# Kernel optimization log

Measured on AMD Instinct MI355X. Metric: run time of the kernel, lower is better.

The kernel has to match this reference:

```python
import jax, jax.numpy as jnp
import numpy as np

N0 = 4096
C = 128
DEPTH = 3
RATIO = 0.5
AVG_DEG = 32
BN_EPS = 1e-5


def setup_inputs() -> dict:
    key = jax.random.key(0)
    ks = jax.random.split(key, 6)
    x = jax.random.normal(ks[0], (N0, C), dtype=jnp.float32)
    # sparse symmetric adjacency (avg degree ~AVG_DEG), no self loops, dense layout
    mask = jax.random.bernoulli(ks[1], AVG_DEG / N0, (N0, N0)).astype(jnp.float32)
    adj = jnp.maximum(mask, mask.T) * (1.0 - jnp.eye(N0, dtype=jnp.float32))
    scale = 1.0 / np.sqrt(C)
    conv_w = jax.random.normal(ks[2], (2 * DEPTH + 1, C, C), dtype=jnp.float32) * scale
    conv_b = jax.random.normal(ks[3], (2 * DEPTH + 1, C), dtype=jnp.float32) * 0.01
    pool_w = jax.random.normal(ks[4], (DEPTH, C), dtype=jnp.float32)
    bn_g = jnp.ones((2 * DEPTH + 1, C), dtype=jnp.float32)
    bn_b = jnp.zeros((2 * DEPTH + 1, C), dtype=jnp.float32)
    return {"x": x, "adj": adj, "conv_w": conv_w, "conv_b": conv_b,
            "pool_w": pool_w, "bn_g": bn_g, "bn_b": bn_b}


def _gcn(x, A, W, b):
    # GCNConv(improved=True): A_hat = A + 2I, symmetric deg normalization
    n = A.shape[0]
    Ah = A + 2.0 * jnp.eye(n, dtype=A.dtype)
    deg = Ah.sum(axis=1)
    d_safe = jnp.where(deg > 0, deg, 1.0)
    dn = jnp.where(deg > 0, jax.lax.rsqrt(d_safe), 0.0)
    An = dn[:, None] * Ah * dn[None, :]
    return An @ (x @ W) + b


def _bn(x, g, b):
    # BatchNorm1d, training mode (biased variance)
    m = x.mean(axis=0)
    v = x.var(axis=0)
    return g * (x - m) * jax.lax.rsqrt(v + BN_EPS) + b


def _augment(A):
    # add_self_loops -> spspmm(A,A) -> remove_self_loops, done densely
    n = A.shape[0]
    I = jnp.eye(n, dtype=A.dtype)
    Aa = A + I
    return (Aa @ Aa) * (1.0 - I)


def _topk_pool(x, A, p):
    score = jnp.tanh((x @ p) / jnp.linalg.norm(p))
    k = int(np.ceil(RATIO * x.shape[0]))
    vals, perm = jax.lax.top_k(score, k)
    xn = x[perm] * vals[:, None]
    An = A[perm][:, perm]
    return xn, An, perm


def reference(x, adj, conv_w, conv_b, pool_w, bn_g, bn_b):
    x = x.astype(jnp.float32)
    x = _bn(jax.nn.relu(_gcn(x, adj, conv_w[0], conv_b[0])), bn_g[0], bn_b[0])
    xs, adjs, perms = [x], [adj], []
    A = adj
    for i in range(1, DEPTH + 1):
        A2 = _augment(A)
        x, A, perm = _topk_pool(x, A2, pool_w[i - 1])
        x = _bn(jax.nn.relu(_gcn(x, A, conv_w[i], conv_b[i])), bn_g[i], bn_b[i])
        if i < DEPTH:
            xs.append(x)
            adjs.append(A)
        perms.append(perm)
    for i in range(DEPTH):
        j = DEPTH - 1 - i
        res, Aj, perm = xs[j], adjs[j], perms[j]
        up = jnp.zeros_like(res).at[perm].set(x)
        x = res + up  # sum_res=True
        x = _gcn(x, Aj, conv_w[DEPTH + 1 + i], conv_b[DEPTH + 1 + i])
        if i < DEPTH - 1:
            x = jax.nn.relu(x)
        x = _bn(x, bn_g[DEPTH + 1 + i], bn_b[DEPTH + 1 + i])
    return x
```

## Files before the change

### kernel.cpp

```cpp
#include <hip/hip_runtime.h>
#include <cstdint>
#include <cstddef>

typedef __bf16 bf16;
typedef __bf16 bf16x8 __attribute__((ext_vector_type(8)));
typedef __bf16 bf16x4 __attribute__((ext_vector_type(4)));
typedef float floatx4 __attribute__((ext_vector_type(4)));
typedef int   intx4  __attribute__((ext_vector_type(4)));
typedef short shortx8 __attribute__((ext_vector_type(8)));
typedef char  cx8    __attribute__((ext_vector_type(8)));

#define GLD16(gp, lp) __builtin_amdgcn_global_load_lds( \
    (const __attribute__((address_space(1))) void*)(gp), \
    (__attribute__((address_space(3))) void*)(lp), 16, 0, 0)

__global__ __launch_bounds__(256) void gemm_sym_i8(
    const char* __restrict__ R, short* __restrict__ Cs16, int* __restrict__ Cs32,
    int n , int kIters, int G, int pairs)
{
  __shared__ __align__(16) char As[128 * 64];
  __shared__ __align__(16) char Bs[128 * 64];

  const int pair = blockIdx.x;
  int rem = pair, bm = 0;
  while (rem >= G - bm) { rem -= G - bm; ++bm; }
  const int bn = bm + rem;
  const int m0 = bm * 128;
  const int n0 = bn * 128;

  const int t = threadIdx.x;
  const int w = t >> 6, l = t & 63;
  const int wr = w >> 1, wc = w & 1;
  const int lr = l & 15, q = l >> 4;
  const int k0base = blockIdx.y * kIters * 64;

  const char* Ab = R + (size_t)m0 * n + k0base;
  const char* Bb = R + (size_t)n0 * n + k0base;
  const int srow = t >> 2;
  const int schunk = (t & 3) * 16;

  intx4 acc[4][4];
#pragma unroll
  for (int i = 0; i < 4; ++i)
#pragma unroll
    for (int j = 0; j < 4; ++j) acc[i][j] = (intx4)0;

  for (int kb = 0; kb < kIters; ++kb) {
    const int k0 = kb * 64;
    __syncthreads();
    GLD16(Ab + (size_t)srow * n + k0 + schunk,        As + (size_t)t * 16);
    GLD16(Ab + (size_t)(srow + 64) * n + k0 + schunk, As + (size_t)(t + 256) * 16);
    GLD16(Bb + (size_t)srow * n + k0 + schunk,        Bs + (size_t)t * 16);
    GLD16(Bb + (size_t)(srow + 64) * n + k0 + schunk, Bs + (size_t)(t + 256) * 16);
    __syncthreads();

    intx4 af[4], bfr[4];
#pragma unroll
    for (int mi = 0; mi < 4; ++mi)
      af[mi] = *(const intx4*)&As[(wr * 64 + mi * 16 + lr) * 64 + q * 16];
#pragma unroll
    for (int ni = 0; ni < 4; ++ni)
      bfr[ni] = *(const intx4*)&Bs[(wc * 64 + ni * 16 + lr) * 64 + q * 16];
#pragma unroll
    for (int mi = 0; mi < 4; ++mi)
#pragma unroll
      for (int ni = 0; ni < 4; ++ni)
        acc[mi][ni] = __builtin_amdgcn_mfma_i32_16x16x64_i8(
            af[mi], bfr[ni], acc[mi][ni], 0, 0, 0);
  }

  const size_t so = ((size_t)blockIdx.y * pairs + pair) * 16384;
#pragma unroll
  for (int mi = 0; mi < 4; ++mi)
#pragma unroll
    for (int ni = 0; ni < 4; ++ni) {
      const int cl = wc * 64 + ni * 16 + lr;
      const int rb = wr * 64 + mi * 16 + q * 4;
#pragma unroll
      for (int r = 0; r < 4; ++r) {
        int v = acc[mi][ni][r];
        if (Cs16) Cs16[so + (size_t)(rb + r) * 128 + cl] = (short)v;
        else      Cs32[so + (size_t)(rb + r) * 128 + cl] = v;
      }
    }
}

__global__ void sym_post_i(const short* __restrict__ Cs16, const int* __restrict__ Cs32,
                           bf16* __restrict__ Abf, float* __restrict__ Af,
                           int k, int G, int pairs, int nz)
{
  int rem = blockIdx.x, bm = 0;
  while (rem >= G - bm) { rem -= G - bm; ++bm; }
  const int bn = bm + rem;
  const int t = threadIdx.x;
  const int i = t >> 1;
  const int jc = blockIdx.y * 16 + (t & 1) * 8;
  const int r = bm * 128 + i;
  const size_t sbase = (size_t)blockIdx.x * 16384 + (size_t)i * 128 + jc;

  int v[8];
#pragma unroll
  for (int e = 0; e < 8; ++e) v[e] = 0;
  for (int z = 0; z < nz; ++z) {
    const size_t off = sbase + (size_t)z * pairs * 16384;
    if (Cs16) {
      shortx8 a = *(const shortx8*)&Cs16[off];
#pragma unroll
      for (int e = 0; e < 8; ++e) v[e] += (int)a[e];
    } else {
      intx4 a0 = *(const intx4*)&Cs32[off];
      intx4 a1 = *(const intx4*)&Cs32[off + 4];
#pragma unroll
      for (int e = 0; e < 4; ++e) { v[e] += a0[e]; v[e + 4] += a1[e]; }
    }
  }
#pragma unroll
  for (int e = 0; e < 8; ++e) {
    const int c = bn * 128 + jc + e;
    const float val = (c == r) ? 0.0f : (float)v[e];
    if (Abf) Abf[(size_t)r * k + c] = (bf16)val;
    if (Af)  Af[(size_t)r * k + c] = val;
    if (bm != bn) {
      if (Abf) Abf[(size_t)c * k + r] = (bf16)val;
      if (Af)  Af[(size_t)c * k + r] = val;
    }
  }
}

__global__ __launch_bounds__(256) void gemm_sym(
    const bf16* __restrict__ R, bf16* __restrict__ CsBf, float* __restrict__ CsF,
    int n , int kIters, int G, int pairs)
{
  __shared__ __align__(16) bf16 As[128 * 32];
  __shared__ __align__(16) bf16 Bs[128 * 32];

  const int pair = blockIdx.x;
  int rem = pair, bm = 0;
  while (rem >= G - bm) { rem -= G - bm; ++bm; }
  const int bn = bm + rem;
  const int m0 = bm * 128;
  const int n0 = bn * 128;

  const int t = threadIdx.x;
  const int w = t >> 6, l = t & 63;
  const int wr = w >> 1, wc = w & 1;
  const int lr = l & 15, q = l >> 4;
  const int k0base = blockIdx.y * kIters * 32;

  const bf16* Ab = R + (size_t)m0 * n + k0base;
  const bf16* Bb = R + (size_t)n0 * n + k0base;
  const int srow = t >> 2;
  const int schunk = (t & 3) * 8;

  floatx4 acc[4][4];
#pragma unroll
  for (int i = 0; i < 4; ++i)
#pragma unroll
    for (int j = 0; j < 4; ++j) acc[i][j] = (floatx4)0.0f;

  for (int kb = 0; kb < kIters; ++kb) {
    const int k0 = kb * 32;
    __syncthreads();
    GLD16(Ab + (size_t)srow * n + k0 + schunk,        As + (size_t)t * 8);
    GLD16(Ab + (size_t)(srow + 64) * n + k0 + schunk, As + (size_t)(t + 256) * 8);
    GLD16(Bb + (size_t)srow * n + k0 + schunk,        Bs + (size_t)t * 8);
    GLD16(Bb + (size_t)(srow + 64) * n + k0 + schunk, Bs + (size_t)(t + 256) * 8);
    __syncthreads();

    bf16x8 af[4], bfr[4];
#pragma unroll
    for (int mi = 0; mi < 4; ++mi)
      af[mi] = *(const bf16x8*)&As[(wr * 64 + mi * 16 + lr) * 32 + q * 8];
#pragma unroll
    for (int ni = 0; ni < 4; ++ni)
      bfr[ni] = *(const bf16x8*)&Bs[(wc * 64 + ni * 16 + lr) * 32 + q * 8];
#pragma unroll
    for (int mi = 0; mi < 4; ++mi)
#pragma unroll
      for (int ni = 0; ni < 4; ++ni)
        acc[mi][ni] = __builtin_amdgcn_mfma_f32_16x16x32_bf16(
            af[mi], bfr[ni], acc[mi][ni], 0, 0, 0);
  }

  const size_t so = ((size_t)blockIdx.y * pairs + pair) * 16384;
#pragma unroll
  for (int mi = 0; mi < 4; ++mi)
#pragma unroll
    for (int ni = 0; ni < 4; ++ni) {
      const int cl = wc * 64 + ni * 16 + lr;
      const int rb = wr * 64 + mi * 16 + q * 4;
#pragma unroll
      for (int r = 0; r < 4; ++r) {
        float v = acc[mi][ni][r];
        if (CsBf) CsBf[so + (size_t)(rb + r) * 128 + cl] = (bf16)v;
        else      CsF[so + (size_t)(rb + r) * 128 + cl] = v;
      }
    }
}

__global__ void sym_post(const bf16* __restrict__ CsBf, const float* __restrict__ CsF,
                         bf16* __restrict__ Abf, float* __restrict__ Af,
                         int k, int G, int pairs, int nz)
{
  int rem = blockIdx.x, bm = 0;
  while (rem >= G - bm) { rem -= G - bm; ++bm; }
  const int bn = bm + rem;
  const int t = threadIdx.x;
  const int i = t >> 1;
  const int jc = blockIdx.y * 16 + (t & 1) * 8;
  const int r = bm * 128 + i;
  const size_t sbase = (size_t)blockIdx.x * 16384 + (size_t)i * 128 + jc;

  float v[8];
#pragma unroll
  for (int e = 0; e < 8; ++e) v[e] = 0.0f;
  for (int z = 0; z < nz; ++z) {
    const size_t off = sbase + (size_t)z * pairs * 16384;
    if (CsBf) {
      bf16x8 a = *(const bf16x8*)&CsBf[off];
#pragma unroll
      for (int e = 0; e < 8; ++e) v[e] += (float)a[e];
    } else {
#pragma unroll
      for (int e = 0; e < 8; e += 4) {
        floatx4 a = *(const floatx4*)&CsF[off + e];
#pragma unroll
        for (int j = 0; j < 4; ++j) v[e + j] += a[j];
      }
    }
  }
#pragma unroll
  for (int e = 0; e < 8; ++e) {
    const int c = bn * 128 + jc + e;
    const float val = (c == r) ? 0.0f : v[e];
    if (Abf) Abf[(size_t)r * k + c] = (bf16)val;
    if (Af)  Af[(size_t)r * k + c] = val;
    if (bm != bn) {
      if (Abf) Abf[(size_t)c * k + r] = (bf16)val;
      if (Af)  Af[(size_t)c * k + r] = val;
    }
  }
}

template <int NP>
__global__ __launch_bounds__(256) void agg_bf(
    const bf16* __restrict__ A, int lda,
    const bf16* __restrict__ Zh, const bf16* __restrict__ Zm, const bf16* __restrict__ Zl,
    int ldz, float* __restrict__ Y, int kIters)
{
  __shared__ __align__(16) bf16 As[64 * 32];
  __shared__ __align__(16) bf16 Zs[NP][128 * 32];

  const int t = threadIdx.x;
  const int w = t >> 6, l = t & 63;
  const int wr = w >> 1, wc = w & 1;
  const int lr = l & 15, q = l >> 4;
  const int m0 = blockIdx.x * 64;
  const int k0base = blockIdx.y * kIters * 32;

  const int srow = t >> 2;
  const int schunk = (t & 3) * 8;

  floatx4 acc[2][4];
#pragma unroll
  for (int i = 0; i < 2; ++i)
#pragma unroll
    for (int j = 0; j < 4; ++j) acc[i][j] = (floatx4)0.0f;

  for (int kb = 0; kb < kIters; ++kb) {
    const int k0 = k0base + kb * 32;
    __syncthreads();
    GLD16(A + (size_t)(m0 + srow) * lda + k0 + schunk, As + (size_t)t * 8);
    GLD16(Zh + (size_t)srow * ldz + k0 + schunk,        Zs[0] + (size_t)t * 8);
    GLD16(Zh + (size_t)(srow + 64) * ldz + k0 + schunk, Zs[0] + (size_t)(t + 256) * 8);
    GLD16(Zm + (size_t)srow * ldz + k0 + schunk,        Zs[1] + (size_t)t * 8);
    GLD16(Zm + (size_t)(srow + 64) * ldz + k0 + schunk, Zs[1] + (size_t)(t + 256) * 8);
    if (NP > 2) {
      GLD16(Zl + (size_t)srow * ldz + k0 + schunk,        Zs[2] + (size_t)t * 8);
      GLD16(Zl + (size_t)(srow + 64) * ldz + k0 + schunk, Zs[2] + (size_t)(t + 256) * 8);
    }
    __syncthreads();

    bf16x8 af[2], bz[NP][4];
#pragma unroll
    for (int mi = 0; mi < 2; ++mi)
      af[mi] = *(const bf16x8*)&As[(wr * 32 + mi * 16 + lr) * 32 + q * 8];
#pragma unroll
    for (int s = 0; s < NP; ++s)
#pragma unroll
      for (int ni = 0; ni < 4; ++ni)
        bz[s][ni] = *(const bf16x8*)&Zs[s][(wc * 64 + ni * 16 + lr) * 32 + q * 8];
#pragma unroll
    for (int s = 0; s < NP; ++s)
#pragma unroll
      for (int mi = 0; mi < 2; ++mi)
#pragma unroll
        for (int ni = 0; ni < 4; ++ni)
          acc[mi][ni] = __builtin_amdgcn_mfma_f32_16x16x32_bf16(
              af[mi], bz[s][ni], acc[mi][ni], 0, 0, 0);
  }

#pragma unroll
  for (int mi = 0; mi < 2; ++mi)
#pragma unroll
    for (int ni = 0; ni < 4; ++ni) {
      const int col = wc * 64 + ni * 16 + lr;
      const int rowb = m0 + wr * 32 + mi * 16 + q * 4;
#pragma unroll
      for (int r = 0; r < 4; ++r)
        atomicAdd(&Y[(size_t)(rowb + r) * 128 + col], acc[mi][ni][r]);
    }
}

template <int NP>
__global__ __launch_bounds__(256) void agg_split(
    const float* __restrict__ A, int lda,
    const bf16* __restrict__ Zh, const bf16* __restrict__ Zm, const bf16* __restrict__ Zl,
    int ldz, float* __restrict__ Y, int kIters, int aTwo)
{
  __shared__ __align__(16) bf16 Ahs[64 * 32];
  __shared__ __align__(16) bf16 Als[64 * 32];
  __shared__ __align__(16) bf16 Zs[NP][128 * 32];

  const int t = threadIdx.x;
  const int w = t >> 6, l = t & 63;
  const int wr = w >> 1, wc = w & 1;
  const int lr = l & 15, q = l >> 4;
  const int m0 = blockIdx.x * 64;
  const int k0base = blockIdx.y * kIters * 32;

  const int arow = t >> 2;
  const int acol = (t & 3) * 8;
  const int srow = t >> 2;
  const int schunk = (t & 3) * 8;

  floatx4 acc[2][4];
#pragma unroll
  for (int i = 0; i < 2; ++i)
#pragma unroll
    for (int j = 0; j < 4; ++j) acc[i][j] = (floatx4)0.0f;

  for (int kb = 0; kb < kIters; ++kb) {
    const int k0 = k0base + kb * 32;
    const float* asrc = A + (size_t)(m0 + arow) * lda + k0 + acol;
    floatx4 av[2];
#pragma unroll
    for (int i = 0; i < 2; ++i) av[i] = *(const floatx4*)(asrc + i * 4);

    __syncthreads();
    GLD16(Zh + (size_t)srow * ldz + k0 + schunk,        Zs[0] + (size_t)t * 8);
    GLD16(Zh + (size_t)(srow + 64) * ldz + k0 + schunk, Zs[0] + (size_t)(t + 256) * 8);
    GLD16(Zm + (size_t)srow * ldz + k0 + schunk,        Zs[1] + (size_t)t * 8);
    GLD16(Zm + (size_t)(srow + 64) * ldz + k0 + schunk, Zs[1] + (size_t)(t + 256) * 8);
    if (NP > 2) {
      GLD16(Zl + (size_t)srow * ldz + k0 + schunk,        Zs[2] + (size_t)t * 8);
      GLD16(Zl + (size_t)(srow + 64) * ldz + k0 + schunk, Zs[2] + (size_t)(t + 256) * 8);
    }

    bf16x4 ah[2], alo[2];
    const int grow = m0 + arow;
#pragma unroll
    for (int i = 0; i < 8; ++i) {
      float v = av[i >> 2][i & 3];
      if (k0 + acol + i == grow) v = 0.0f;
      bf16 h = (bf16)v;
      ah[i >> 2][i & 3] = h;
      alo[i >> 2][i & 3] = (bf16)(v - (float)h);
    }
    const int sbase = arow * 32 + acol;
    *(bf16x4*)&Ahs[sbase] = ah[0]; *(bf16x4*)&Ahs[sbase + 4] = ah[1];
    if (aTwo) { *(bf16x4*)&Als[sbase] = alo[0]; *(bf16x4*)&Als[sbase + 4] = alo[1]; }
    __syncthreads();

    bf16x8 afh[2], afl[2], bz[NP][4];
#pragma unroll
    for (int mi = 0; mi < 2; ++mi)
      afh[mi] = *(const bf16x8*)&Ahs[(wr * 32 + mi * 16 + lr) * 32 + q * 8];
#pragma unroll
    for (int s = 0; s < NP; ++s)
#pragma unroll
      for (int ni = 0; ni < 4; ++ni)
        bz[s][ni] = *(const bf16x8*)&Zs[s][(wc * 64 + ni * 16 + lr) * 32 + q * 8];
#pragma unroll
    for (int s = 0; s < NP; ++s)
#pragma unroll
      for (int mi = 0; mi < 2; ++mi)
#pragma unroll
        for (int ni = 0; ni < 4; ++ni)
          acc[mi][ni] = __builtin_amdgcn_mfma_f32_16x16x32_bf16(
              afh[mi], bz[s][ni], acc[mi][ni], 0, 0, 0);
    if (aTwo) {
#pragma unroll
      for (int mi = 0; mi < 2; ++mi)
        afl[mi] = *(const bf16x8*)&Als[(wr * 32 + mi * 16 + lr) * 32 + q * 8];
      constexpr int NL = (NP > 2) ? 2 : 1;
#pragma unroll
      for (int s = 0; s < NL; ++s)
#pragma unroll
        for (int mi = 0; mi < 2; ++mi)
#pragma unroll
          for (int ni = 0; ni < 4; ++ni)
            acc[mi][ni] = __builtin_amdgcn_mfma_f32_16x16x32_bf16(
                afl[mi], bz[s][ni], acc[mi][ni], 0, 0, 0);
    }
  }

#pragma unroll
  for (int mi = 0; mi < 2; ++mi)
#pragma unroll
    for (int ni = 0; ni < 4; ++ni) {
      const int col = wc * 64 + ni * 16 + lr;
      const int rowb = m0 + wr * 32 + mi * 16 + q * 4;
#pragma unroll
      for (int r = 0; r < 4; ++r)
        atomicAdd(&Y[(size_t)(rowb + r) * 128 + col], acc[mi][ni][r]);
    }
}

template <int FULL>
__global__ __launch_bounds__(256) void xw_split(
    const float* __restrict__ X, const int* __restrict__ perm,
    const float* __restrict__ vals,
    const float* __restrict__ up, const int* __restrict__ inv,
    const float* __restrict__ statsP, const float* __restrict__ gP,
    const float* __restrict__ bP, float nP,
    const bf16* __restrict__ Wh, const bf16* __restrict__ Wm, const bf16* __restrict__ Wl,
    const float* __restrict__ dnv, float* __restrict__ Z,
    bf16* __restrict__ Zht, bf16* __restrict__ Zmt, bf16* __restrict__ Zlt, int ldz,
    float* __restrict__ Agg, float* __restrict__ stats)
{
  __shared__ __align__(16) bf16 Xs[3][128 * 32];
  __shared__ __align__(16) bf16 Ws[3][128 * 32];
  __shared__ float scU[128], offU[128];

  const int t = threadIdx.x;
  if (blockIdx.x == 0) stats[t] = 0.0f;

  const int w = t >> 6, l = t & 63;
  const int wr = w >> 1, wc = w & 1;
  const int lr = l & 15, q = l >> 4;
  const int r0 = blockIdx.x * 128;

  const int srow = t >> 1;
  const int soff = (t & 1) * 16;
  const int sbase = srow * 32 + soff;

  if (statsP) {
    if (t < 128) {
      float m = statsP[t] / nP;
      float var = statsP[128 + t] / nP - m * m;
      float sc = gP[t] / sqrtf(var + 1e-5f);
      scU[t] = sc;
      offU[t] = bP[t] - m * sc;
    }
    __syncthreads();
  }

  const int row = r0 + srow;
  int grow = row;
  float scale = 1.0f;
  if (perm) { grow = perm[row]; scale = vals[row]; }
  const float* xrow = X + (size_t)grow * 128;
  const float* uprow = nullptr;
  if (up) { int j = inv[row]; if (j >= 0) uprow = up + (size_t)j * 128; }

  floatx4 acc[4][4];
#pragma unroll
  for (int i = 0; i < 4; ++i)
#pragma unroll
    for (int j = 0; j < 4; ++j) acc[i][j] = (floatx4)0.0f;

  const bf16* wsrc[3] = {Wh, Wm, Wl};

  for (int ks = 0; ks < 4; ++ks) {
    const int k0 = ks * 32;
    float xv[16];
#pragma unroll
    for (int i = 0; i < 16; i += 4) {
      floatx4 tmp = *(const floatx4*)(xrow + k0 + soff + i);
      if (uprow) {
        floatx4 u = *(const floatx4*)(uprow + k0 + soff + i);
        if (statsP) {
#pragma unroll
          for (int j = 0; j < 4; ++j) {
            const int c = k0 + soff + i + j;
            u[j] = scU[c] * u[j] + offU[c];
          }
        }
        tmp += u;
      }
      xv[i] = tmp[0] * scale; xv[i + 1] = tmp[1] * scale;
      xv[i + 2] = tmp[2] * scale; xv[i + 3] = tmp[3] * scale;
    }
    bf16x8 wv[3][2];
#pragma unroll
    for (int s = 0; s < 3; ++s) {
      const bf16* ws = wsrc[s] + (size_t)srow * 128 + k0 + soff;
      wv[s][0] = *(const bf16x8*)ws;
      wv[s][1] = *(const bf16x8*)(ws + 8);
    }
    bf16x8 vh[2], vm[2], vl[2];
#pragma unroll
    for (int i = 0; i < 16; ++i) {
      float v = xv[i];
      bf16 h = (bf16)v; float r1 = v - (float)h;
      bf16 m = (bf16)r1; float r2 = r1 - (float)m;
      vh[i >> 3][i & 7] = h; vm[i >> 3][i & 7] = m; vl[i >> 3][i & 7] = (bf16)r2;
    }
    __syncthreads();
    *(bf16x8*)&Xs[0][sbase] = vh[0]; *(bf16x8*)&Xs[0][sbase + 8] = vh[1];
    *(bf16x8*)&Xs[1][sbase] = vm[0]; *(bf16x8*)&Xs[1][sbase + 8] = vm[1];
    *(bf16x8*)&Xs[2][sbase] = vl[0]; *(bf16x8*)&Xs[2][sbase + 8] = vl[1];
#pragma unroll
    for (int s = 0; s < 3; ++s) {
      *(bf16x8*)&Ws[s][sbase] = wv[s][0];
      *(bf16x8*)&Ws[s][sbase + 8] = wv[s][1];
    }
    __syncthreads();

    bf16x8 af[3][4], bfg[3][4];
#pragma unroll
    for (int s = 0; s < 3; ++s) {
#pragma unroll
      for (int mi = 0; mi < 4; ++mi)
        af[s][mi] = *(const bf16x8*)&Xs[s][(wr * 64 + mi * 16 + lr) * 32 + q * 8];
#pragma unroll
      for (int ni = 0; ni < 4; ++ni)
        bfg[s][ni] = *(const bf16x8*)&Ws[s][(wc * 64 + ni * 16 + lr) * 32 + q * 8];
    }
    constexpr int NT = FULL ? 6 : 3;
    constexpr int sa[6] = {0, 0, 1, 1, 0, 2};
    constexpr int sb[6] = {0, 1, 0, 1, 2, 0};
#pragma unroll
    for (int p = 0; p < NT; ++p)
#pragma unroll
      for (int mi = 0; mi < 4; ++mi)
#pragma unroll
        for (int ni = 0; ni < 4; ++ni)
          acc[mi][ni] = __builtin_amdgcn_mfma_f32_16x16x32_bf16(
              af[sa[p]][mi], bfg[sb[p]][ni], acc[mi][ni], 0, 0, 0);
  }

#pragma unroll
  for (int mi = 0; mi < 4; ++mi) {
    const int rowb = r0 + wr * 64 + mi * 16 + q * 4;
    float dnr[4];
#pragma unroll
    for (int r = 0; r < 4; ++r) dnr[r] = dnv[rowb + r];
#pragma unroll
    for (int ni = 0; ni < 4; ++ni) {
      const int col = wc * 64 + ni * 16 + lr;
      bf16x4 h4, m4, l4;
#pragma unroll
      for (int r = 0; r < 4; ++r) {
        float v = dnr[r] * acc[mi][ni][r];
        Z[(size_t)(rowb + r) * 128 + col] = v;
        Agg[(size_t)(rowb + r) * 128 + col] = 0.0f;
        bf16 h = (bf16)v; float r1 = v - (float)h;
        bf16 m = (bf16)r1; float r2 = r1 - (float)m;
        h4[r] = h; m4[r] = m; l4[r] = (bf16)r2;
      }
      *(bf16x4*)&Zht[(size_t)col * ldz + rowb] = h4;
      *(bf16x4*)&Zmt[(size_t)col * ldz + rowb] = m4;
      if (FULL) *(bf16x4*)&Zlt[(size_t)col * ldz + rowb] = l4;
    }
  }
}

__global__ void prep_all(const float* __restrict__ adj, bf16* __restrict__ ah,
                         float* __restrict__ dn, int n,
                         const float* __restrict__ W, bf16* __restrict__ Wh,
                         bf16* __restrict__ Wm, bf16* __restrict__ Wl,
                         const float* __restrict__ pw, float* __restrict__ invp) {
  const int bid = blockIdx.x;
  const int t = threadIdx.x;
  if (bid < 4096) {
    int r = bid;
    const float* arow = adj + (size_t)r * n;
    bf16* orow = ah + (size_t)r * n;
    float sum = 0.f;
    for (int c4 = t * 4; c4 < n; c4 += 1024) {
      floatx4 v = *(const floatx4*)(arow + c4);
      bf16x4 o;
#pragma unroll
      for (int e = 0; e < 4; ++e) {
        float x = (c4 + e == r) ? 0.0f : v[e];
        sum += x; o[e] = (bf16)x;
      }
      *(bf16x4*)&orow[c4] = o;
    }
    __shared__ float red[256];
    red[t] = sum; __syncthreads();
    for (int off = 128; off; off >>= 1) {
      if (t < off) red[t] += red[t + off];
      __syncthreads();
    }
    if (t == 0) dn[r] = 1.0f / sqrtf(red[0] + 2.0f);
  } else if (bid < 4544) {
    int idx = (bid - 4096) * 256 + t;
    int l = idx >> 14, rem = idx & 16383, c = rem >> 7, k = rem & 127;
    float v = W[(l << 14) + (k << 7) + c];
    bf16 h = (bf16)v; float r1 = v - (float)h;
    bf16 m = (bf16)r1; float r2 = r1 - (float)m;
    Wh[idx] = h; Wm[idx] = m; Wl[idx] = (bf16)r2;
  } else {
    __shared__ float red[128];
    if (t < 128) {
      for (int l = 0; l < 3; ++l) {
        float v = pw[l * 128 + t];
        red[t] = v * v; __syncthreads();
        for (int off = 64; off; off >>= 1) {
          if (t < off) red[t] += red[t + off];
          __syncthreads();
        }
        if (t == 0) invp[l] = 1.0f / sqrtf(red[0]);
        __syncthreads();
      }
    }
  }
}

__global__ void dn_rows_bf(const bf16* __restrict__ A, int lda, float* __restrict__ dn,
                           int n) {
  int r = blockIdx.x, t = threadIdx.x;
  const bf16* row = A + (size_t)r * lda;
  float sum = 0.f;
  for (int c4 = t * 4; c4 < n; c4 += 1024) {
    bf16x4 v = *(const bf16x4*)&row[c4];
#pragma unroll
    for (int e = 0; e < 4; ++e) sum += (float)v[e];
  }
  __shared__ float red[256];
  red[t] = sum; __syncthreads();
  for (int off = 128; off; off >>= 1) {
    if (t < off) red[t] += red[t + off];
    __syncthreads();
  }
  if (t == 0) dn[r] = 1.0f / sqrtf(red[0] + 2.0f);
}

__global__ void dn_rows(const float* __restrict__ A, int lda, float* __restrict__ dn,
                        int n) {
  int r = blockIdx.x, t = threadIdx.x;
  const float* row = A + (size_t)r * lda;
  float sum = 0.f;
  for (int c = t; c < n; c += 256)
    if (c != r) sum += row[c];
  __shared__ float red[256];
  red[t] = sum; __syncthreads();
  for (int off = 128; off; off >>= 1) {
    if (t < off) red[t] += red[t + off];
    __syncthreads();
  }
  if (t == 0) dn[r] = 1.0f / sqrtf(red[0] + 2.0f);
}

__device__ inline unsigned f2u(float f) {
  unsigned u = __float_as_uint(f);
  return (u & 0x80000000u) ? ~u : (u | 0x80000000u);
}
__global__ __launch_bounds__(1024) void select_kernel(
    const float* __restrict__ s, int n, int k,
    int* __restrict__ perm, float* __restrict__ vals, int* __restrict__ inv)
{
  __shared__ int hist[256];
  __shared__ unsigned sh_prefix;
  __shared__ int sh_krem;
  __shared__ float sh_thr;
  __shared__ int wsum[16];
  __shared__ int wgs[16], wes[16];
  const int t = threadIdx.x;
  const int lane = t & 63;
  const int wid = t >> 6;
  if (t == 0) { sh_prefix = 0; sh_krem = k; }

  for (int round = 0; round < 4; ++round) {
    const int shift = 24 - 8 * round;
    if (t < 256) hist[t] = 0;
    __syncthreads();
    const unsigned pref = sh_prefix;
    const int krem = sh_krem;
    for (int i = t; i < n; i += 1024) {
      unsigned u = f2u(s[i]);
      if (round == 0 || (u >> (shift + 8)) == pref)
        atomicAdd(&hist[(u >> shift) & 255], 1);
    }
    __syncthreads();
    int v = 0, own = 0;
    if (t < 256) {
      own = hist[255 - t];
      v = own;
#pragma unroll
      for (int off = 1; off < 64; off <<= 1) {
        int u = __shfl_up(v, off, 64);
        if (lane >= off) v += u;
      }
      if (lane == 63) wsum[wid] = v;
    }
    __syncthreads();
    if (t < 256) {
      int add = 0;
      for (int wi = 0; wi < wid; ++wi) add += wsum[wi];
      v += add;
      const int prev = v - own;
      if (v >= krem && prev < krem) {
        sh_prefix = (pref << 8) | (unsigned)(255 - t);
        sh_krem = krem - prev;
      }
    }
    __syncthreads();
  }
  if (t == 0) {
    unsigned u = sh_prefix;
    sh_thr = (u & 0x80000000u) ? __uint_as_float(u & 0x7fffffffu)
                               : __uint_as_float(~u);
  }
  for (int i = t; i < n; i += 1024) inv[i] = -1;
  __syncthreads();

  const float thr = sh_thr;
  const int chunk = n >> 10;
  const int beg = t * chunk;
  int g = 0, e = 0;
  for (int i = 0; i < chunk; ++i) {
    float v = s[beg + i];
    g += (v > thr); e += (v == thr);
  }
  int vg = g, ve = e;
#pragma unroll
  for (int off = 1; off < 64; off <<= 1) {
    int ug = __shfl_up(vg, off, 64);
    int ue = __shfl_up(ve, off, 64);
    if (lane >= off) { vg += ug; ve += ue; }
  }
  if (lane == 63) { wgs[wid] = vg; wes[wid] = ve; }
  __syncthreads();
  int ag = 0, ae = 0;
  for (int wi = 0; wi < wid; ++wi) { ag += wgs[wi]; ae += wes[wi]; }
  int total_gt = 0;
#pragma unroll
  for (int wi = 0; wi < 16; ++wi) total_gt += wgs[wi];
  int pg = vg + ag - g;
  int pe = ve + ae - e;
  const int need = k - total_gt;
  for (int i = 0; i < chunk; ++i) {
    float v = s[beg + i];
    if (v > thr) {
      if (pg < k) { perm[pg] = beg + i; vals[pg] = v; inv[beg + i] = pg; }
      ++pg;
    } else if (v == thr) {
      if (pe < need && total_gt + pe < k) {
        perm[total_gt + pe] = beg + i; vals[total_gt + pe] = v;
        inv[beg + i] = total_gt + pe;
      }
      ++pe;
    }
  }
}

__global__ void gather_i8(const bf16* __restrict__ src, int lda,
                          const int* __restrict__ perm, char* __restrict__ R, int n) {
  int j = blockIdx.x, t = threadIdx.x;
  int r = perm[j];
  const bf16* s = src + (size_t)r * lda;
  char* o = R + (size_t)j * n;
  for (int c = t * 8; c < n; c += 2048) {
    bf16x8 v = *(const bf16x8*)&s[c];
    cx8 ob;
#pragma unroll
    for (int e = 0; e < 8; ++e)
      ob[e] = (c + e == r) ? (char)1 : (char)(float)v[e];
    *(cx8*)&o[c] = ob;
  }
}

__global__ void gather_f32(const float* __restrict__ src, int lda,
                           const int* __restrict__ perm, bf16* __restrict__ R, int n) {
  int j = blockIdx.x, t = threadIdx.x;
  int r = perm[j];
  const float* s = src + (size_t)r * lda;
  bf16* o = R + (size_t)j * n;
  for (int c4 = t * 4; c4 < n; c4 += 1024) {
    floatx4 v = *(const floatx4*)(s + c4);
    bf16x4 ob;
#pragma unroll
    for (int e = 0; e < 4; ++e)
      ob[e] = (c4 + e == r) ? (bf16)1.0f : (bf16)v[e];
    *(bf16x4*)&o[c4] = ob;
  }
}

__global__ void gcn_post(float* __restrict__ acc, const float* __restrict__ Zf,
                         const float* __restrict__ dn, const float* __restrict__ bias,
                         float* __restrict__ stats, int relu,
                         float* __restrict__ hout) {
  int c = threadIdx.x;
  int r0 = blockIdx.x * 16;
  float b = bias[c];
  float s = 0.f, qq = 0.f;
  for (int i = 0; i < 16; ++i) {
    int r = r0 + i;
    float v = dn[r] * (acc[(size_t)r * 128 + c] + 2.0f * Zf[(size_t)r * 128 + c]) + b;
    if (relu) v = fmaxf(v, 0.f);
    hout[(size_t)r * 128 + c] = v;
    s += v; qq += v * v;
  }
  atomicAdd(&stats[c], s);
  atomicAdd(&stats[128 + c], qq);
}

__global__ void bn_apply(const float* __restrict__ H, const float* __restrict__ stats,
                         const float* __restrict__ g, const float* __restrict__ b,
                         int n, float* __restrict__ xout,
                         const float* __restrict__ pw, const float* __restrict__ invp,
                         float* __restrict__ scores) {
  int r = blockIdx.x, c = threadIdx.x;
  float m = stats[c] / n;
  float var = stats[128 + c] / n - m * m;
  float sc = g[c] / sqrtf(var + 1e-5f);
  float off = b[c] - m * sc;
  float v = sc * H[(size_t)r * 128 + c] + off;
  xout[(size_t)r * 128 + c] = v;
  if (pw) {
    __shared__ float red[128];
    red[c] = v * pw[c]; __syncthreads();
    for (int o = 64; o; o >>= 1) {
      if (c < o) red[c] += red[c + o];
      __syncthreads();
    }
    if (c == 0) scores[r] = tanhf(red[0] * invp[0]);
  }
}

extern "C" void kernel_launch(void* const* d_in, const int* in_sizes, int n_in,
                              void* d_out, int out_size, void* d_ws, size_t ws_size,
                              hipStream_t stream) {
  const float* x_in   = (const float*)d_in[0];
  const float* adj    = (const float*)d_in[1];
  const float* conv_w = (const float*)d_in[2];
  const float* conv_b = (const float*)d_in[3];
  const float* pool_w = (const float*)d_in[4];
  const float* bn_g   = (const float*)d_in[5];
  const float* bn_b   = (const float*)d_in[6];
  float* out = (float*)d_out;
  (void)in_sizes; (void)n_in; (void)out_size; (void)ws_size;

  char* p = (char*)d_ws;
  auto alloc = [&](size_t bytes) -> void* {
    void* r = (void*)p;
    p += (bytes + 255) & ~(size_t)255;
    return r;
  };
  bf16*  Ah0bf = (bf16*)alloc(4096ull * 4096 * 2);
  bf16*  A1bf  = (bf16*)alloc(2048ull * 2048 * 2);
  float* A2f   = (float*)alloc(1024ull * 1024 * 4);
  float* A3f   = (float*)alloc(512ull * 512 * 4);
  char*  Rbuf  = (char*)alloc(2048ull * 4096 * 2);
  void*  Cs    = alloc(40ull << 20);
  float* Z     = (float*)alloc(4096ull * 128 * 4);
  bf16*  Zht   = (bf16*)alloc(128ull * 4096 * 2);
  bf16*  Zmt   = (bf16*)alloc(128ull * 4096 * 2);
  bf16*  Zlt   = (bf16*)alloc(128ull * 4096 * 2);
  float* Agg   = (float*)alloc(4096ull * 128 * 4);
  float* res0  = (float*)alloc(4096ull * 128 * 4);
  float* res1  = (float*)alloc(2048ull * 128 * 4);
  float* res2  = (float*)alloc(1024ull * 128 * 4);
  float* xb0   = (float*)alloc(512ull * 128 * 4);
  float* xb1   = (float*)alloc(1024ull * 128 * 4);
  float* xb2   = (float*)alloc(2048ull * 128 * 4);
  bf16*  Wh    = (bf16*)alloc(7ull * 16384 * 2);
  bf16*  Wm    = (bf16*)alloc(7ull * 16384 * 2);
  bf16*  Wl    = (bf16*)alloc(7ull * 16384 * 2);
  float* scores = (float*)alloc(4096 * 4);
  int*   perm0 = (int*)alloc(2048 * 4);
  int*   perm1 = (int*)alloc(1024 * 4);
  int*   perm2 = (int*)alloc(512 * 4);
  int*   inv0  = (int*)alloc(4096 * 4);
  int*   inv1  = (int*)alloc(2048 * 4);
  int*   inv2  = (int*)alloc(1024 * 4);
  float* vals0 = (float*)alloc(2048 * 4);
  float* vals1 = (float*)alloc(1024 * 4);
  float* vals2 = (float*)alloc(512 * 4);
  float* dn0   = (float*)alloc(4096 * 4);
  float* dn1   = (float*)alloc(2048 * 4);
  float* dn2   = (float*)alloc(1024 * 4);
  float* dn3   = (float*)alloc(512 * 4);
  float* invp  = (float*)alloc(256);
  float* stats = (float*)alloc(7ull * 256 * 4);

  auto gcn = [&](int nr, const bf16* Abf, const float* Af32, const float* dnv,
                 int layer, const float* xsrc, const int* perm, const float* vals,
                 const float* up, const int* inv, float* xout, int relu, int aTwo,
                 const float* pw, const float* ip, int full,
                 const float* statsP, const float* gP, const float* bPv, float nP,
                 int doBn) {
    float* st = stats + layer * 256;
    if (full)
      xw_split<1><<<nr / 128, 256, 0, stream>>>(
          xsrc, perm, vals, up, inv, statsP, gP, bPv, nP,
          Wh + layer * 16384, Wm + layer * 16384, Wl + layer * 16384, dnv,
          Z, Zht, Zmt, Zlt, nr, Agg, st);
    else
      xw_split<0><<<nr / 128, 256, 0, stream>>>(
          xsrc, perm, vals, up, inv, statsP, gP, bPv, nP,
          Wh + layer * 16384, Wm + layer * 16384, Wl + layer * 16384, dnv,
          Z, Zht, Zmt, Zlt, nr, Agg, st);
    if (Abf) {
      if (full)
        agg_bf<3><<<dim3(nr / 64, 8), 256, 0, stream>>>(
            Abf, nr, Zht, Zmt, Zlt, nr, Agg, nr / 256);
      else
        agg_bf<2><<<dim3(nr / 64, 8), 256, 0, stream>>>(
            Abf, nr, Zht, Zmt, Zlt, nr, Agg, nr / 256);
    } else {
      if (full)
        agg_split<3><<<dim3(nr / 64, 8), 256, 0, stream>>>(
            Af32, nr, Zht, Zmt, Zlt, nr, Agg, nr / 256, aTwo);
      else
        agg_split<2><<<dim3(nr / 64, 8), 256, 0, stream>>>(
            Af32, nr, Zht, Zmt, Zlt, nr, Agg, nr / 256, aTwo);
    }
    gcn_post<<<nr / 16, 128, 0, stream>>>(Agg, Z, dnv, conv_b + layer * 128, st, relu,
                                          doBn ? Agg : xout);
    if (doBn)
      bn_apply<<<nr, 128, 0, stream>>>(Agg, st, bn_g + layer * 128, bn_b + layer * 128,
                                       nr, xout, pw, ip, scores);
  };

  auto pool = [&](int n, const bf16* srcBf, const float* srcF32,
                  bf16* outBf, float* outF32, float* dnNew,
                  int* perm, float* vals, int* inv, int splitZ, int mode) {
    int k = n / 2, G = k / 128, pairs = G * (G + 1) / 2;
    select_kernel<<<1, 1024, 0, stream>>>(scores, n, k, perm, vals, inv);
    if (mode <= 1) {
      gather_i8<<<k, 256, 0, stream>>>(srcBf, n, perm, Rbuf, n);
      gemm_sym_i8<<<dim3(pairs, splitZ), 256, 0, stream>>>(
          Rbuf, mode == 0 ? (short*)Cs : nullptr, mode == 0 ? nullptr : (int*)Cs,
          n, n / (splitZ * 64), G, pairs);
      sym_post_i<<<dim3(pairs, 8), 256, 0, stream>>>(
          mode == 0 ? (const short*)Cs : nullptr, mode == 0 ? nullptr : (const int*)Cs,
          outBf, outF32, k, G, pairs, splitZ);
    } else {
      gather_f32<<<k, 256, 0, stream>>>(srcF32, n, perm, (bf16*)Rbuf, n);
      gemm_sym<<<dim3(pairs, splitZ), 256, 0, stream>>>(
          (const bf16*)Rbuf, nullptr, (float*)Cs, n, n / (splitZ * 32), G, pairs);
      sym_post<<<dim3(pairs, 8), 256, 0, stream>>>(
          nullptr, (const float*)Cs, outBf, outF32, k, G, pairs, splitZ);
    }
    if (outBf) dn_rows_bf<<<k, 256, 0, stream>>>(outBf, k, dnNew, k);
    else       dn_rows<<<k, 256, 0, stream>>>(outF32, k, dnNew, k);
  };

  prep_all<<<4545, 256, 0, stream>>>(adj, Ah0bf, dn0, 4096,
                                     conv_w, Wh, Wm, Wl, pool_w, invp);

  gcn(4096, Ah0bf, nullptr, dn0, 0, x_in, nullptr, nullptr, nullptr, nullptr,
      res0, 1, 0, pool_w + 0, invp + 0, 1, nullptr, nullptr, nullptr, 1.0f, 1);
  pool(4096, Ah0bf, nullptr, A1bf, nullptr, dn1, perm0, vals0, inv0, 4, 0);
  gcn(2048, A1bf, nullptr, dn1, 1, res0, perm0, vals0, nullptr, nullptr,
      res1, 1, 0, pool_w + 128, invp + 1, 1, nullptr, nullptr, nullptr, 1.0f, 1);
  pool(2048, A1bf, nullptr, nullptr, A2f, dn2, perm1, vals1, inv1, 8, 1);
  gcn(1024, nullptr, A2f, dn2, 2, res1, perm1, vals1, nullptr, nullptr,
      res2, 1, 1, pool_w + 256, invp + 2, 1, nullptr, nullptr, nullptr, 1.0f, 1);
  pool(1024, nullptr, A2f, nullptr, A3f, dn3, perm2, vals2, inv2, 8, 2);
  gcn(512, nullptr, A3f, dn3, 3, res2, perm2, vals2, nullptr, nullptr,
      xb0, 1, 1, nullptr, nullptr, 0, nullptr, nullptr, nullptr, 1.0f, 0);

  gcn(1024, nullptr, A2f, dn2, 4, res2, nullptr, nullptr, xb0, inv2,
      xb1, 1, 1, nullptr, nullptr, 0,
      stats + 3 * 256, bn_g + 3 * 128, bn_b + 3 * 128, 512.0f, 0);
  gcn(2048, A1bf, nullptr, dn1, 5, res1, nullptr, nullptr, xb1, inv1,
      xb2, 1, 0, nullptr, nullptr, 0,
      stats + 4 * 256, bn_g + 4 * 128, bn_b + 4 * 128, 1024.0f, 0);
  gcn(4096, Ah0bf, nullptr, dn0, 6, res0, nullptr, nullptr, xb2, inv0,
      out, 0, 0, nullptr, nullptr, 0,
      stats + 5 * 256, bn_g + 5 * 128, bn_b + 5 * 128, 2048.0f, 1);
}
```

Measured before the change: 510.2 us.

## Store small adjacency matrices as int8 and fuse degree sums into sym_post

The level-0 and level-1 adjacency matrices are now stored as int8 instead of bf16, which halves their memory footprint and the bytes read by aggregation and gather. The aggregation kernel loads int8 rows and converts them to bf16 in registers before writing to LDS, in place of an async global-to-LDS copy. Row degree sums are accumulated with atomics inside the sym_post kernels, which removes the separate dn_rows passes. The rsqrt step moves to the consumers. The int8 path assumes level-1 entries fit in a signed char, and the float atomics make the degree sums order-dependent.

```diff
diff --git a/kernel.cpp b/kernel.cpp
--- a/kernel.cpp
+++ b/kernel.cpp
@@ -8,7 +8,9 @@
 typedef float floatx4 __attribute__((ext_vector_type(4)));
 typedef int   intx4  __attribute__((ext_vector_type(4)));
 typedef short shortx8 __attribute__((ext_vector_type(8)));
+typedef char  cx4    __attribute__((ext_vector_type(4)));
 typedef char  cx8    __attribute__((ext_vector_type(8)));
+typedef char  cx16   __attribute__((ext_vector_type(16)));
 
 #define GLD16(gp, lp) __builtin_amdgcn_global_load_lds( \
     (const __attribute__((address_space(1))) void*)(gp), \
@@ -86,9 +88,11 @@
 }
 
 __global__ void sym_post_i(const short* __restrict__ Cs16, const int* __restrict__ Cs32,
-                           bf16* __restrict__ Abf, float* __restrict__ Af,
+                           char* __restrict__ Ai8, float* __restrict__ Af,
+                           float* __restrict__ dnS,
                            int k, int G, int pairs, int nz)
 {
+  __shared__ float colS[16];
   int rem = blockIdx.x, bm = 0;
   while (rem >= G - bm) { rem -= G - bm; ++bm; }
   const int bn = bm + rem;
@@ -98,6 +102,9 @@
   const int r = bm * 128 + i;
   const size_t sbase = (size_t)blockIdx.x * 16384 + (size_t)i * 128 + jc;
 
+  if (t < 16) colS[t] = 0.0f;
+  __syncthreads();
+
   int v[8];
 #pragma unroll
   for (int e = 0; e < 8; ++e) v[e] = 0;
@@ -114,17 +121,25 @@
       for (int e = 0; e < 4; ++e) { v[e] += a0[e]; v[e + 4] += a1[e]; }
     }
   }
+  float rs = 0.0f;
 #pragma unroll
   for (int e = 0; e < 8; ++e) {
     const int c = bn * 128 + jc + e;
-    const float val = (c == r) ? 0.0f : (float)v[e];
-    if (Abf) Abf[(size_t)r * k + c] = (bf16)val;
-    if (Af)  Af[(size_t)r * k + c] = val;
+    const int val = (c == r) ? 0 : v[e];
+    const float valf = (float)val;
+    rs += valf;
+    if (Ai8) Ai8[(size_t)r * k + c] = (char)val;
+    if (Af)  Af[(size_t)r * k + c] = valf;
     if (bm != bn) {
-      if (Abf) Abf[(size_t)c * k + r] = (bf16)val;
-      if (Af)  Af[(size_t)c * k + r] = val;
-    }
-  }
+      if (Ai8) Ai8[(size_t)c * k + r] = (char)val;
+      if (Af)  Af[(size_t)c * k + r] = valf;
+      atomicAdd(&colS[(t & 1) * 8 + e], valf);
+    }
+  }
+  atomicAdd(&dnS[r], rs);
+  __syncthreads();
+  if (bm != bn && t < 16)
+    atomicAdd(&dnS[bn * 128 + blockIdx.y * 16 + t], colS[t]);
 }
 
 __global__ __launch_bounds__(256) void gemm_sym(
@@ -198,10 +213,11 @@
     }
 }
 
-__global__ void sym_post(const bf16* __restrict__ CsBf, const float* __restrict__ CsF,
-                         bf16* __restrict__ Abf, float* __restrict__ Af,
+__global__ void sym_post(const float* __restrict__ CsF,
+                         float* __restrict__ Af, float* __restrict__ dnS,
                          int k, int G, int pairs, int nz)
 {
+  __shared__ float colS[16];
   int rem = blockIdx.x, bm = 0;
   while (rem >= G - bm) { rem -= G - bm; ++bm; }
   const int bn = bm + rem;
@@ -211,40 +227,42 @@
   const int r = bm * 128 + i;
   const size_t sbase = (size_t)blockIdx.x * 16384 + (size_t)i * 128 + jc;
 
+  if (t < 16) colS[t] = 0.0f;
+  __syncthreads();
+
   float v[8];
 #pragma unroll
   for (int e = 0; e < 8; ++e) v[e] = 0.0f;
   for (int z = 0; z < nz; ++z) {
     const size_t off = sbase + (size_t)z * pairs * 16384;
-    if (CsBf) {
-      bf16x8 a = *(const bf16x8*)&CsBf[off];
-#pragma unroll
-      for (int e = 0; e < 8; ++e) v[e] += (float)a[e];
-    } else {
-#pragma unroll
-      for (int e = 0; e < 8; e += 4) {
-        floatx4 a = *(const floatx4*)&CsF[off + e];
-#pragma unroll
-        for (int j = 0; j < 4; ++j) v[e + j] += a[j];
-      }
-    }
-  }
+#pragma unroll
+    for (int e = 0; e < 8; e += 4) {
+      floatx4 a = *(const floatx4*)&CsF[off + e];
+#pragma unroll
+      for (int j = 0; j < 4; ++j) v[e + j] += a[j];
+    }
+  }
+  float rs = 0.0f;
 #pragma unroll
   for (int e = 0; e < 8; ++e) {
     const int c = bn * 128 + jc + e;
     const float val = (c == r) ? 0.0f : v[e];
-    if (Abf) Abf[(size_t)r * k + c] = (bf16)val;
-    if (Af)  Af[(size_t)r * k + c] = val;
+    rs += val;
+    Af[(size_t)r * k + c] = val;
     if (bm != bn) {
-      if (Abf) Abf[(size_t)c * k + r] = (bf16)val;
-      if (Af)  Af[(size_t)c * k + r] = val;
-    }
-  }
+      Af[(size_t)c * k + r] = val;
+      atomicAdd(&colS[(t & 1) * 8 + e], val);
+    }
+  }
+  atomicAdd(&dnS[r], rs);
+  __syncthreads();
+  if (bm != bn && t < 16)
+    atomicAdd(&dnS[bn * 128 + blockIdx.y * 16 + t], colS[t]);
 }
 
 template <int NP>
-__global__ __launch_bounds__(256) void agg_bf(
-    const bf16* __restrict__ A, int lda,
+__global__ __launch_bounds__(256) void agg_i8(
+    const char* __restrict__ A, int lda,
     const bf16* __restrict__ Zh, const bf16* __restrict__ Zm, const bf16* __restrict__ Zl,
     int ldz, float* __restrict__ Y, int kIters)
 {
@@ -258,6 +276,8 @@
   const int m0 = blockIdx.x * 64;
   const int k0base = blockIdx.y * kIters * 32;
 
+  const int arow = t >> 2;
+  const int acol = (t & 3) * 8;
   const int srow = t >> 2;
   const int schunk = (t & 3) * 8;
 
@@ -269,8 +289,9 @@
 
   for (int kb = 0; kb < kIters; ++kb) {
     const int k0 = k0base + kb * 32;
-    __syncthreads();
-    GLD16(A + (size_t)(m0 + srow) * lda + k0 + schunk, As + (size_t)t * 8);
+    cx8 av = *(const cx8*)(A + (size_t)(m0 + arow) * lda + k0 + acol);
+
+    __syncthreads();
     GLD16(Zh + (size_t)srow * ldz + k0 + schunk,        Zs[0] + (size_t)t * 8);
     GLD16(Zh + (size_t)(srow + 64) * ldz + k0 + schunk, Zs[0] + (size_t)(t + 256) * 8);
     GLD16(Zm + (size_t)srow * ldz + k0 + schunk,        Zs[1] + (size_t)t * 8);
@@ -279,6 +300,11 @@
       GLD16(Zl + (size_t)srow * ldz + k0 + schunk,        Zs[2] + (size_t)t * 8);
       GLD16(Zl + (size_t)(srow + 64) * ldz + k0 + schunk, Zs[2] + (size_t)(t + 256) * 8);
     }
+
+    bf16x8 ab;
+#pragma unroll
+    for (int i = 0; i < 8; ++i) ab[i] = (bf16)(float)(int)av[i];
+    *(bf16x8*)&As[arow * 32 + acol] = ab;
     __syncthreads();
 
     bf16x8 af[2], bz[NP][4];
@@ -546,7 +572,7 @@
     const int rowb = r0 + wr * 64 + mi * 16 + q * 4;
     float dnr[4];
 #pragma unroll
-    for (int r = 0; r < 4; ++r) dnr[r] = dnv[rowb + r];
+    for (int r = 0; r < 4; ++r) dnr[r] = 1.0f / sqrtf(dnv[rowb + r] + 2.0f);
 #pragma unroll
     for (int ni = 0; ni < 4; ++ni) {
       const int col = wc * 64 + ni * 16 + lr;
@@ -567,7 +593,7 @@
   }
 }
 
-__global__ void prep_all(const float* __restrict__ adj, bf16* __restrict__ ah,
+__global__ void prep_all(const float* __restrict__ adj, char* __restrict__ ah,
                          float* __restrict__ dn, int n,
                          const float* __restrict__ W, bf16* __restrict__ Wh,
                          bf16* __restrict__ Wm, bf16* __restrict__ Wl,
@@ -577,17 +603,17 @@
   if (bid < 4096) {
     int r = bid;
     const float* arow = adj + (size_t)r * n;
-    bf16* orow = ah + (size_t)r * n;
+    char* orow = ah + (size_t)r * n;
     float sum = 0.f;
     for (int c4 = t * 4; c4 < n; c4 += 1024) {
       floatx4 v = *(const floatx4*)(arow + c4);
-      bf16x4 o;
+      cx4 o;
 #pragma unroll
       for (int e = 0; e < 4; ++e) {
         float x = (c4 + e == r) ? 0.0f : v[e];
-        sum += x; o[e] = (bf16)x;
+        sum += x; o[e] = (char)x;
       }
-      *(bf16x4*)&orow[c4] = o;
+      *(cx4*)&orow[c4] = o;
     }
     __shared__ float red[256];
     red[t] = sum; __syncthreads();
@@ -595,7 +621,7 @@
       if (t < off) red[t] += red[t + off];
       __syncthreads();
     }
-    if (t == 0) dn[r] = 1.0f / sqrtf(red[0] + 2.0f);
+    if (t == 0) dn[r] = red[0];
   } else if (bid < 4544) {
     int idx = (bid - 4096) * 256 + t;
     int l = idx >> 14, rem = idx & 16383, c = rem >> 7, k = rem & 127;
@@ -620,41 +646,6 @@
   }
 }
 
-__global__ void dn_rows_bf(const bf16* __restrict__ A, int lda, float* __restrict__ dn,
-                           int n) {
-  int r = blockIdx.x, t = threadIdx.x;
-  const bf16* row = A + (size_t)r * lda;
-  float sum = 0.f;
-  for (int c4 = t * 4; c4 < n; c4 += 1024) {
-    bf16x4 v = *(const bf16x4*)&row[c4];
-#pragma unroll
-    for (int e = 0; e < 4; ++e) sum += (float)v[e];
-  }
-  __shared__ float red[256];
-  red[t] = sum; __syncthreads();
-  for (int off = 128; off; off >>= 1) {
-    if (t < off) red[t] += red[t + off];
-    __syncthreads();
-  }
-  if (t == 0) dn[r] = 1.0f / sqrtf(red[0] + 2.0f);
-}
-
-__global__ void dn_rows(const float* __restrict__ A, int lda, float* __restrict__ dn,
-                        int n) {
-  int r = blockIdx.x, t = threadIdx.x;
-  const float* row = A + (size_t)r * lda;
-  float sum = 0.f;
-  for (int c = t; c < n; c += 256)
-    if (c != r) sum += row[c];
-  __shared__ float red[256];
-  red[t] = sum; __syncthreads();
-  for (int off = 128; off; off >>= 1) {
-    if (t < off) red[t] += red[t + off];
-    __syncthreads();
-  }
-  if (t == 0) dn[r] = 1.0f / sqrtf(red[0] + 2.0f);
-}
-
 __device__ inline unsigned f2u(float f) {
   unsigned u = __float_as_uint(f);
   return (u & 0x80000000u) ? ~u : (u | 0x80000000u);
@@ -758,26 +749,27 @@
   }
 }
 
-__global__ void gather_i8(const bf16* __restrict__ src, int lda,
-                          const int* __restrict__ perm, char* __restrict__ R, int n) {
+__global__ void gather_i8(const char* __restrict__ src, int lda,
+                          const int* __restrict__ perm, char* __restrict__ R, int n,
+                          float* __restrict__ dnz) {
   int j = blockIdx.x, t = threadIdx.x;
   int r = perm[j];
-  const bf16* s = src + (size_t)r * lda;
+  if (t == 0) dnz[j] = 0.0f;
+  const char* s = src + (size_t)r * lda;
   char* o = R + (size_t)j * n;
-  for (int c = t * 8; c < n; c += 2048) {
-    bf16x8 v = *(const bf16x8*)&s[c];
-    cx8 ob;
-#pragma unroll
-    for (int e = 0; e < 8; ++e)
-      ob[e] = (c + e == r) ? (char)1 : (char)(float)v[e];
-    *(cx8*)&o[c] = ob;
+  for (int c = t * 16; c < n; c += 4096) {
+    cx16 v = *(const cx16*)&s[c];
+    if (r >= c && r < c + 16) v[r - c] = (char)1;
+    *(cx16*)&o[c] = v;
   }
 }
 
 __global__ void gather_f32(const float* __restrict__ src, int lda,
-                           const int* __restrict__ perm, bf16* __restrict__ R, int n) {
+                           const int* __restrict__ perm, bf16* __restrict__ R, int n,
+                           float* __restrict__ dnz) {
   int j = blockIdx.x, t = threadIdx.x;
   int r = perm[j];
+  if (t == 0) dnz[j] = 0.0f;
   const float* s = src + (size_t)r * lda;
   bf16* o = R + (size_t)j * n;
   for (int c4 = t * 4; c4 < n; c4 += 1024) {
@@ -800,7 +792,8 @@
   float s = 0.f, qq = 0.f;
   for (int i = 0; i < 16; ++i) {
     int r = r0 + i;
-    float v = dn[r] * (acc[(size_t)r * 128 + c] + 2.0f * Zf[(size_t)r * 128 + c]) + b;
+    float d = 1.0f / sqrtf(dn[r] + 2.0f);
+    float v = d * (acc[(size_t)r * 128 + c] + 2.0f * Zf[(size_t)r * 128 + c]) + b;
     if (relu) v = fmaxf(v, 0.f);
     hout[(size_t)r * 128 + c] = v;
     s += v; qq += v * v;
@@ -851,8 +844,8 @@
     p += (bytes + 255) & ~(size_t)255;
     return r;
   };
-  bf16*  Ah0bf = (bf16*)alloc(4096ull * 4096 * 2);
-  bf16*  A1bf  = (bf16*)alloc(2048ull * 2048 * 2);
+  char*  Ah0i8 = (char*)alloc(4096ull * 4096);
+  char*  A1i8  = (char*)alloc(2048ull * 2048);
   float* A2f   = (float*)alloc(1024ull * 1024 * 4);
   float* A3f   = (float*)alloc(512ull * 512 * 4);
   char*  Rbuf  = (char*)alloc(2048ull * 4096 * 2);
@@ -888,7 +881,7 @@
   float* invp  = (float*)alloc(256);
   float* stats = (float*)alloc(7ull * 256 * 4);
 
-  auto gcn = [&](int nr, const bf16* Abf, const float* Af32, const float* dnv,
+  auto gcn = [&](int nr, const char* Ai8, const float* Af32, const float* dnv,
                  int layer, const float* xsrc, const int* perm, const float* vals,
                  const float* up, const int* inv, float* xout, int relu, int aTwo,
                  const float* pw, const float* ip, int full,
@@ -905,13 +898,13 @@
           xsrc, perm, vals, up, inv, statsP, gP, bPv, nP,
           Wh + layer * 16384, Wm + layer * 16384, Wl + layer * 16384, dnv,
           Z, Zht, Zmt, Zlt, nr, Agg, st);
-    if (Abf) {
+    if (Ai8) {
       if (full)
-        agg_bf<3><<<dim3(nr / 64, 8), 256, 0, stream>>>(
-            Abf, nr, Zht, Zmt, Zlt, nr, Agg, nr / 256);
+        agg_i8<3><<<dim3(nr / 64, 8), 256, 0, stream>>>(
+            Ai8, nr, Zht, Zmt, Zlt, nr, Agg, nr / 256);
       else
-        agg_bf<2><<<dim3(nr / 64, 8), 256, 0, stream>>>(
-            Abf, nr, Zht, Zmt, Zlt, nr, Agg, nr / 256);
+        agg_i8<2><<<dim3(nr / 64, 8), 256, 0, stream>>>(
+            Ai8, nr, Zht, Zmt, Zlt, nr, Agg, nr / 256);
     } else {
       if (full)
         agg_split<3><<<dim3(nr / 64, 8), 256, 0, stream>>>(
@@ -927,39 +920,37 @@
                                        nr, xout, pw, ip, scores);
   };
 
-  auto pool = [&](int n, const bf16* srcBf, const float* srcF32,
-                  bf16* outBf, float* outF32, float* dnNew,
+  auto pool = [&](int n, const char* srcI8, const float* srcF32,
+                  char* outI8, float* outF32, float* dnNew,
                   int* perm, float* vals, int* inv, int splitZ, int mode) {
     int k = n / 2, G = k / 128, pairs = G * (G + 1) / 2;
     select_kernel<<<1, 1024, 0, stream>>>(scores, n, k, perm, vals, inv);
     if (mode <= 1) {
-      gather_i8<<<k, 256, 0, stream>>>(srcBf, n, perm, Rbuf, n);
+      gather_i8<<<k, 256, 0, stream>>>(srcI8, n, perm, Rbuf, n, dnNew);
       gemm_sym_i8<<<dim3(pairs, splitZ), 256, 0, stream>>>(
           Rbuf, mode == 0 ? (short*)Cs : nullptr, mode == 0 ? nullptr : (int*)Cs,
           n, n / (splitZ * 64), G, pairs);
       sym_post_i<<<dim3(pairs, 8), 256, 0, stream>>>(
           mode == 0 ? (const short*)Cs : nullptr, mode == 0 ? nullptr : (const int*)Cs,
-          outBf, outF32, k, G, pairs, splitZ);
+          outI8, outF32, dnNew, k, G, pairs, splitZ);
     } else {
-      gather_f32<<<k, 256, 0, stream>>>(srcF32, n, perm, (bf16*)Rbuf, n);
+      gather_f32<<<k, 256, 0, stream>>>(srcF32, n, perm, (bf16*)Rbuf, n, dnNew);
       gemm_sym<<<dim3(pairs, splitZ), 256, 0, stream>>>(
           (const bf16*)Rbuf, nullptr, (float*)Cs, n, n / (splitZ * 32), G, pairs);
       sym_post<<<dim3(pairs, 8), 256, 0, stream>>>(
-          nullptr, (const float*)Cs, outBf, outF32, k, G, pairs, splitZ);
-    }
-    if (outBf) dn_rows_bf<<<k, 256, 0, stream>>>(outBf, k, dnNew, k);
-    else       dn_rows<<<k, 256, 0, stream>>>(outF32, k, dnNew, k);
+          (const float*)Cs, outF32, dnNew, k, G, pairs, splitZ);
+    }
   };
 
-  prep_all<<<4545, 256, 0, stream>>>(adj, Ah0bf, dn0, 4096,
+  prep_all<<<4545, 256, 0, stream>>>(adj, Ah0i8, dn0, 4096,
                                      conv_w, Wh, Wm, Wl, pool_w, invp);
 
-  gcn(4096, Ah0bf, nullptr, dn0, 0, x_in, nullptr, nullptr, nullptr, nullptr,
+  gcn(4096, Ah0i8, nullptr, dn0, 0, x_in, nullptr, nullptr, nullptr, nullptr,
       res0, 1, 0, pool_w + 0, invp + 0, 1, nullptr, nullptr, nullptr, 1.0f, 1);
-  pool(4096, Ah0bf, nullptr, A1bf, nullptr, dn1, perm0, vals0, inv0, 4, 0);
-  gcn(2048, A1bf, nullptr, dn1, 1, res0, perm0, vals0, nullptr, nullptr,
+  pool(4096, Ah0i8, nullptr, A1i8, nullptr, dn1, perm0, vals0, inv0, 4, 0);
+  gcn(2048, A1i8, nullptr, dn1, 1, res0, perm0, vals0, nullptr, nullptr,
       res1, 1, 0, pool_w + 128, invp + 1, 1, nullptr, nullptr, nullptr, 1.0f, 1);
-  pool(2048, A1bf, nullptr, nullptr, A2f, dn2, perm1, vals1, inv1, 8, 1);
+  pool(2048, A1i8, nullptr, nullptr, A2f, dn2, perm1, vals1, inv1, 8, 1);
   gcn(1024, nullptr, A2f, dn2, 2, res1, perm1, vals1, nullptr, nullptr,
       res2, 1, 1, pool_w + 256, invp + 2, 1, nullptr, nullptr, nullptr, 1.0f, 1);
   pool(1024, nullptr, A2f, nullptr, A3f, dn3, perm2, vals2, inv2, 8, 2);
@@ -969,10 +960,10 @@
   gcn(1024, nullptr, A2f, dn2, 4, res2, nullptr, nullptr, xb0, inv2,
       xb1, 1, 1, nullptr, nullptr, 0,
       stats + 3 * 256, bn_g + 3 * 128, bn_b + 3 * 128, 512.0f, 0);
-  gcn(2048, A1bf, nullptr, dn1, 5, res1, nullptr, nullptr, xb1, inv1,
+  gcn(2048, A1i8, nullptr, dn1, 5, res1, nullptr, nullptr, xb1, inv1,
       xb2, 1, 0, nullptr, nullptr, 0,
       stats + 4 * 256, bn_g + 4 * 128, bn_b + 4 * 128, 1024.0f, 0);
-  gcn(4096, Ah0bf, nullptr, dn0, 6, res0, nullptr, nullptr, xb2, inv0,
+  gcn(4096, Ah0i8, nullptr, dn0, 6, res0, nullptr, nullptr, xb2, inv0,
       out, 0, 0, nullptr, nullptr, 0,
       stats + 5 * 256, bn_g + 5 * 128, bn_b + 5 * 128, 2048.0f, 1);
 }
```

After: 567.5 us. 1.11x slower.
